# Optimization experiments

Hardware: AMD Instinct MI355X
Metric: run time of the kernel (lower is better)

## Reference

```python
import jax, jax.numpy as jnp
import numpy as np
import math

B, T, C = 4, 2048, 1024
H = 128            # num_heads
D = C // H         # head_dim = 8 (n_wires of the quantum device)


def setup_inputs() -> dict:
    key = jax.random.key(0)
    k1, k2, k3 = jax.random.split(key, 3)
    x = jax.random.normal(k1, (B, T, C), dtype=jnp.float32)
    # trainable RX angles: head_dim gates, each a scalar angle (tq.RX has_params=True)
    theta = jax.random.normal(k2, (D,), dtype=jnp.float32)
    # nn.Linear(C, C, bias=False) weight, torch layout [out, in]
    w_proj = jax.random.normal(k3, (C, C), dtype=jnp.float32) / math.sqrt(C)
    return {"x": x, "theta": theta, "w_proj": w_proj}


def _quantum_measure(xh, theta):
    # Circuit per head/token: start |0..0>, apply RX(x_j) on wire j (encoder
    # resets the state each call), then each of the D trainable RX(theta_g)
    # gates is broadcast over all wires. RX angles on one wire compose
    # additively, and <Z> after RX(phi)|0> == cos(phi).
    return jnp.cos(xh + jnp.sum(theta))  # [B, T, H, D]


def reference(x, theta, w_proj):
    xh = x.reshape(B, T, H, D)
    q = _quantum_measure(xh, theta)  # q == k == v (shared encoder + shared gates)
    # torch.matmul on [B,T,H,D]: batch dims (B,T) -> head-vs-head scores [B,T,H,H]
    scores = jnp.einsum('bthd,btgd->bthg', q, q) / math.sqrt(D)
    attn = jax.nn.softmax(scores, axis=-1)  # dropout: identity in eval
    out = jnp.einsum('bthg,btgd->bthd', attn, q).reshape(B, T, C)
    return out @ w_proj.T
```

## Files before the change

### kernel.cpp

```cpp
#include <hip/hip_runtime.h>
#include <hip/hip_bf16.h>
#include <stdint.h>

#define NB 4
#define NT 2048
#define NC 1024
#define NH 128
#define ND 8
#define NTOK (NB*NT)
#define GK 1024
#define GN 1024

typedef __attribute__((ext_vector_type(4))) float f32x4;
typedef __attribute__((ext_vector_type(8))) short bf16x8;
typedef __attribute__((ext_vector_type(8))) _Float16 f16x8;
typedef __attribute__((ext_vector_type(2))) _Float16 f16x2;
typedef __attribute__((ext_vector_type(4))) unsigned int u32x4;
typedef __attribute__((ext_vector_type(2))) unsigned int u32x2;
typedef unsigned int uint32;

#define GAMMA  0.71419167f
#define C1INV  1.4001844f

#define GLOAD_LDS16(g, l) \
  __builtin_amdgcn_global_load_lds((const __attribute__((address_space(1))) void*)(g), \
                                   (__attribute__((address_space(3))) void*)(l), 16, 0, 0)

__device__ __forceinline__ unsigned short f2bf(float f) {
  __bf16 b = (__bf16)f;
  return __builtin_bit_cast(unsigned short, b);
}
__device__ __forceinline__ f16x2 cvtpk_f16(float a, float b) {
  return __builtin_bit_cast(f16x2, __builtin_amdgcn_cvt_pkrtz(a, b));
}

__device__ __forceinline__ uint32 exp2pk(float a, float b) {
  f16x2 s = cvtpk_f16(a, b);
  const f16x2 MAGIC = {(_Float16)1536.0f, (_Float16)1536.0f};
  f16x2 t = s + MAGIC;
  f16x2 f = s - (t - MAGIC);
  const _Float16 k3 = (_Float16)(0.0555041f / 256.0f);
  const _Float16 k2 = (_Float16)(0.2402265f / 256.0f);
  const _Float16 k1 = (_Float16)(0.6931472f / 256.0f);
  const _Float16 k0 = (_Float16)(1.0f / 256.0f);
  const f16x2 P3 = {k3, k3}, P2 = {k2, k2}, P1 = {k1, k1}, P0 = {k0, k0};
  f16x2 p = P2 + f * P3;
  p = P1 + f * p;
  p = P0 + f * p;
  uint32 tb = __builtin_bit_cast(uint32, t);
  uint32 inj = ((((tb << 10) & 0xFC00FC00u) + 0x20002000u) & 0xFC00FC00u);
  return __builtin_bit_cast(uint32, p) + inj;
}

__global__ __launch_bounds__(256) void wconv_kernel(const float4* __restrict__ w,
                                                    ushort4* __restrict__ wb) {
  int i = blockIdx.x * 256 + threadIdx.x;
  float4 v = w[i];
  ushort4 o;
  o.x = f2bf(v.x); o.y = f2bf(v.y); o.z = f2bf(v.z); o.w = f2bf(v.w);
  wb[i] = o;
}

#define QTS 136

__global__ __launch_bounds__(256) void attn_kernel(const float* __restrict__ x,
                                                   const float* __restrict__ theta,
                                                   unsigned short* __restrict__ aout) {
  __shared__ __align__(16) unsigned short QT[4][8 * QTS];

  const int tid = (int)threadIdx.x;
  const int wid = tid >> 6;
  const int tok = blockIdx.x * 4 + wid;
  const int l = tid & 63;
  const int c = l & 15;
  const int t = l >> 4;

  float S = 0.f;
#pragma unroll
  for (int j = 0; j < ND; ++j) S += theta[j];

  u32x4 qf[8];
  unsigned short* qt = &QT[wid][0];
#pragma unroll
  for (int a = 0; a < 8; ++a) {
    float2 xv = *(const float2*)(x + (size_t)tok * NC + (16 * a + c) * ND + 2 * t);
    float q0 = GAMMA * __cosf(xv.x + S);
    float q1 = GAMMA * __cosf(xv.y + S);
    uint32 pk = __builtin_bit_cast(uint32, cvtpk_f16(q0, q1));
    qt[(2 * t) * QTS + 16 * a + c] = (unsigned short)(pk & 0xFFFFu);
    qt[(2 * t + 1) * QTS + 16 * a + c] = (unsigned short)(pk >> 16);
    qf[a].x = pk;
    qf[a].y = 0u; qf[a].z = 0u; qf[a].w = 0u;
  }

  u32x4 bff[4];
  {
    const int cm = (c < 8) ? c : 7;
    const bool isq = (c < 8);
    const uint32 onepair = 0x3C003C00u;
#pragma unroll
    for (int j = 0; j < 4; ++j) {
      u32x2 v0 = *(const u32x2*)&qt[cm * QTS + 32 * j + 4 * t];
      u32x2 v1 = *(const u32x2*)&qt[cm * QTS + 32 * j + 16 + 4 * t];
      bff[j].x = isq ? v0.x : onepair;
      bff[j].y = isq ? v0.y : onepair;
      bff[j].z = isq ? v1.x : onepair;
      bff[j].w = isq ? v1.y : onepair;
    }
  }

  const f32x4 z4 = {0.f, 0.f, 0.f, 0.f};
  unsigned short* orow = aout + (size_t)tok * NC;

#pragma unroll
  for (int b = 0; b < 8; ++b) {
    f32x4 o = z4;
#pragma unroll
    for (int j = 0; j < 4; ++j) {
      f32x4 sv0 = __builtin_amdgcn_mfma_f32_16x16x32_f16(
          __builtin_bit_cast(f16x8, qf[2 * j]), __builtin_bit_cast(f16x8, qf[b]),
          z4, 0, 0, 0);
      f32x4 sv1 = __builtin_amdgcn_mfma_f32_16x16x32_f16(
          __builtin_bit_cast(f16x8, qf[2 * j + 1]), __builtin_bit_cast(f16x8, qf[b]),
          z4, 0, 0, 0);
      u32x4 af;
      af.x = exp2pk(sv0[0], sv0[1]);
      af.y = exp2pk(sv0[2], sv0[3]);
      af.z = exp2pk(sv1[0], sv1[1]);
      af.w = exp2pk(sv1[2], sv1[3]);
      o = __builtin_amdgcn_mfma_f32_16x16x32_f16(
          __builtin_bit_cast(f16x8, af), __builtin_bit_cast(f16x8, bff[j]),
          o, 0, 0, 0);
    }
#pragma unroll
    for (int r = 0; r < 4; ++r) {
      float rs = __shfl_xor(o[r], 8, 64);
      float outv = o[r] * __builtin_amdgcn_rcpf(rs) * C1INV;
      if (c < 8)
        orow[(16 * b + 4 * t + r) * ND + c] = f2bf(outv);
    }
  }
}

#define BM 128
#define BN 128
#define BK 64

__global__ __launch_bounds__(512, 4) void gemm_kernel(const unsigned short* __restrict__ A,
                                                      const unsigned short* __restrict__ Bt,
                                                      float* __restrict__ C) {
  __shared__ __align__(16) unsigned short As[2][BM * BK];
  __shared__ __align__(16) unsigned short Bs[2][BN * BK];

  const int bm = blockIdx.x;
  const int bn = blockIdx.y;
  const int tid = (int)threadIdx.x;
  const int l = tid & 63;
  const int w = tid >> 6;
  const int wm = w >> 2;
  const int wn = w & 3;

  f32x4 acc[4][2] = {};

  const int srow = l >> 3;
  const int schk = (l & 7) ^ srow;
  const unsigned short* gA0 = A + (size_t)(bm * BM + 16 * w + srow) * GK + schk * 8;
  const unsigned short* gA1 = gA0 + 8 * GK;
  const unsigned short* gB0 = Bt + (size_t)(bn * BN + 16 * w + srow) * GK + schk * 8;
  const unsigned short* gB1 = gB0 + 8 * GK;

  const int fr = l & 15;
  const int kcb = l >> 4;
  const int fx = l & 7;

#define STAGE(nb)                                          \
  {                                                        \
    unsigned short* la = &As[nb][(16 * w) * BK];           \
    unsigned short* lb = &Bs[nb][(16 * w) * BK];           \
    GLOAD_LDS16(gA0, la);                                  \
    GLOAD_LDS16(gA1, la + 8 * BK);                         \
    GLOAD_LDS16(gB0, lb);                                  \
    GLOAD_LDS16(gB1, lb + 8 * BK);                         \
    gA0 += BK; gA1 += BK; gB0 += BK; gB1 += BK;            \
  }

  auto compute = [&](const unsigned short* as, const unsigned short* bs) {
#pragma unroll
    for (int s = 0; s < 2; ++s) {
      const int slot = ((4 * s + kcb) ^ fx) * 8;
      bf16x8 af[4], bfr[2];
#pragma unroll
      for (int i = 0; i < 4; ++i)
        af[i] = *reinterpret_cast<const bf16x8*>(&as[(64 * wm + 16 * i + fr) * BK + slot]);
#pragma unroll
      for (int j = 0; j < 2; ++j)
        bfr[j] = *reinterpret_cast<const bf16x8*>(&bs[(32 * wn + 16 * j + fr) * BK + slot]);
#pragma unroll
      for (int i = 0; i < 4; ++i)
#pragma unroll
        for (int j = 0; j < 2; ++j)
          acc[i][j] = __builtin_amdgcn_mfma_f32_16x16x32_bf16(af[i], bfr[j], acc[i][j], 0, 0, 0);
    }
  };

  STAGE(0);

  int buf = 0;
#pragma unroll 1
  for (int t = 0; t < 15; ++t) {
    STAGE(buf ^ 1);
    asm volatile("s_waitcnt vmcnt(4)" ::: "memory");
    __builtin_amdgcn_s_barrier();
    asm volatile("" ::: "memory");
    compute(&As[buf][0], &Bs[buf][0]);
    asm volatile("" ::: "memory");
    __builtin_amdgcn_s_barrier();
    asm volatile("" ::: "memory");
    buf ^= 1;
  }
  asm volatile("s_waitcnt vmcnt(0)" ::: "memory");
  __builtin_amdgcn_s_barrier();
  asm volatile("" ::: "memory");
  compute(&As[1][0], &Bs[1][0]);

  float* Cb = C + (size_t)(bm * BM + 64 * wm) * GN + bn * BN + 32 * wn;
  const int cr = (l >> 4) * 4;
  const int cc = l & 15;
#pragma unroll
  for (int i = 0; i < 4; ++i)
#pragma unroll
    for (int j = 0; j < 2; ++j)
#pragma unroll
      for (int r = 0; r < 4; ++r)
        Cb[(size_t)(16 * i + cr + r) * GN + 16 * j + cc] = acc[i][j][r];
#undef STAGE
}

extern "C" void kernel_launch(void* const* d_in, const int* in_sizes, int n_in,
                              void* d_out, int out_size, void* d_ws, size_t ws_size,
                              hipStream_t stream) {
  (void)in_sizes; (void)n_in; (void)out_size; (void)ws_size;
  const float* x = (const float*)d_in[0];
  const float* theta = (const float*)d_in[1];
  const float* wproj = (const float*)d_in[2];
  float* y = (float*)d_out;

  unsigned short* attn_out = (unsigned short*)d_ws;
  unsigned short* wb = (unsigned short*)((char*)d_ws + (size_t)NTOK * NC * 2);

  wconv_kernel<<<(NC * NC / 4) / 256, 256, 0, stream>>>((const float4*)wproj,
                                                        (ushort4*)wb);
  attn_kernel<<<NTOK / 4, 256, 0, stream>>>(x, theta, attn_out);
  dim3 grid(NTOK / BM, GN / BN);
  gemm_kernel<<<grid, 512, 0, stream>>>(attn_out, wb, y);
}
```

Baseline: 68.76 us.

## Process two tokens per wave in attention kernel with hoisted x loads

Each wave of the attention kernel now handles two tokens, 4096 apart, and issues the global x loads for both before any compute. This raises memory-level parallelism and halves the grid. The score MFMAs are grouped ahead of the exp2 polynomial and the output MFMAs so more independent work is in flight. A min-blocks launch bound of 3 is added. The cost is higher register pressure from holding both tokens' inputs, and the per-wave LDS scratch is reused across the two tokens.

```diff
diff --git a/kernel.cpp b/kernel.cpp
--- a/kernel.cpp
+++ b/kernel.cpp
@@ -63,29 +63,15 @@
 
 #define QTS 136
 
-__global__ __launch_bounds__(256) void attn_kernel(const float* __restrict__ x,
-                                                   const float* __restrict__ theta,
-                                                   unsigned short* __restrict__ aout) {
-  __shared__ __align__(16) unsigned short QT[4][8 * QTS];
-
-  const int tid = (int)threadIdx.x;
-  const int wid = tid >> 6;
-  const int tok = blockIdx.x * 4 + wid;
-  const int l = tid & 63;
-  const int c = l & 15;
-  const int t = l >> 4;
-
-  float S = 0.f;
-#pragma unroll
-  for (int j = 0; j < ND; ++j) S += theta[j];
-
+__device__ __forceinline__ void process_token(const float2* __restrict__ xv,
+                                              float S, unsigned short* qt,
+                                              unsigned short* __restrict__ orow,
+                                              int c, int t) {
   u32x4 qf[8];
-  unsigned short* qt = &QT[wid][0];
 #pragma unroll
   for (int a = 0; a < 8; ++a) {
-    float2 xv = *(const float2*)(x + (size_t)tok * NC + (16 * a + c) * ND + 2 * t);
-    float q0 = GAMMA * __cosf(xv.x + S);
-    float q1 = GAMMA * __cosf(xv.y + S);
+    float q0 = GAMMA * __cosf(xv[a].x + S);
+    float q1 = GAMMA * __cosf(xv[a].y + S);
     uint32 pk = __builtin_bit_cast(uint32, cvtpk_f16(q0, q1));
     qt[(2 * t) * QTS + 16 * a + c] = (unsigned short)(pk & 0xFFFFu);
     qt[(2 * t + 1) * QTS + 16 * a + c] = (unsigned short)(pk >> 16);
@@ -110,28 +96,33 @@
   }
 
   const f32x4 z4 = {0.f, 0.f, 0.f, 0.f};
-  unsigned short* orow = aout + (size_t)tok * NC;
 
 #pragma unroll
   for (int b = 0; b < 8; ++b) {
-    f32x4 o = z4;
+    f32x4 sv[8];
 #pragma unroll
     for (int j = 0; j < 4; ++j) {
-      f32x4 sv0 = __builtin_amdgcn_mfma_f32_16x16x32_f16(
+      sv[2 * j] = __builtin_amdgcn_mfma_f32_16x16x32_f16(
           __builtin_bit_cast(f16x8, qf[2 * j]), __builtin_bit_cast(f16x8, qf[b]),
           z4, 0, 0, 0);
-      f32x4 sv1 = __builtin_amdgcn_mfma_f32_16x16x32_f16(
+      sv[2 * j + 1] = __builtin_amdgcn_mfma_f32_16x16x32_f16(
           __builtin_bit_cast(f16x8, qf[2 * j + 1]), __builtin_bit_cast(f16x8, qf[b]),
           z4, 0, 0, 0);
-      u32x4 af;
-      af.x = exp2pk(sv0[0], sv0[1]);
-      af.y = exp2pk(sv0[2], sv0[3]);
-      af.z = exp2pk(sv1[0], sv1[1]);
-      af.w = exp2pk(sv1[2], sv1[3]);
+    }
+    u32x4 af[4];
+#pragma unroll
+    for (int j = 0; j < 4; ++j) {
+      af[j].x = exp2pk(sv[2 * j][0], sv[2 * j][1]);
+      af[j].y = exp2pk(sv[2 * j][2], sv[2 * j][3]);
+      af[j].z = exp2pk(sv[2 * j + 1][0], sv[2 * j + 1][1]);
+      af[j].w = exp2pk(sv[2 * j + 1][2], sv[2 * j + 1][3]);
+    }
+    f32x4 o = z4;
+#pragma unroll
+    for (int j = 0; j < 4; ++j)
       o = __builtin_amdgcn_mfma_f32_16x16x32_f16(
-          __builtin_bit_cast(f16x8, af), __builtin_bit_cast(f16x8, bff[j]),
+          __builtin_bit_cast(f16x8, af[j]), __builtin_bit_cast(f16x8, bff[j]),
           o, 0, 0, 0);
-    }
 #pragma unroll
     for (int r = 0; r < 4; ++r) {
       float rs = __shfl_xor(o[r], 8, 64);
@@ -140,6 +131,36 @@
         orow[(16 * b + 4 * t + r) * ND + c] = f2bf(outv);
     }
   }
+}
+
+__global__ __launch_bounds__(256, 3) void attn_kernel(const float* __restrict__ x,
+                                                      const float* __restrict__ theta,
+                                                      unsigned short* __restrict__ aout) {
+  __shared__ __align__(16) unsigned short QT[4][8 * QTS];
+
+  const int tid = (int)threadIdx.x;
+  const int wid = tid >> 6;
+  const int tok0 = blockIdx.x * 4 + wid;
+  const int tok1 = tok0 + 4096;
+  const int l = tid & 63;
+  const int c = l & 15;
+  const int t = l >> 4;
+
+  float S = 0.f;
+#pragma unroll
+  for (int j = 0; j < ND; ++j) S += theta[j];
+
+  float2 xv0[8], xv1[8];
+#pragma unroll
+  for (int a = 0; a < 8; ++a)
+    xv0[a] = *(const float2*)(x + (size_t)tok0 * NC + (16 * a + c) * ND + 2 * t);
+#pragma unroll
+  for (int a = 0; a < 8; ++a)
+    xv1[a] = *(const float2*)(x + (size_t)tok1 * NC + (16 * a + c) * ND + 2 * t);
+
+  unsigned short* qt = &QT[wid][0];
+  process_token(xv0, S, qt, aout + (size_t)tok0 * NC, c, t);
+  process_token(xv1, S, qt, aout + (size_t)tok1 * NC, c, t);
 }
 
 #define BM 128
@@ -195,6 +216,7 @@
 #pragma unroll
       for (int j = 0; j < 2; ++j)
         bfr[j] = *reinterpret_cast<const bf16x8*>(&bs[(32 * wn + 16 * j + fr) * BK + slot]);
+
 #pragma unroll
       for (int i = 0; i < 4; ++i)
 #pragma unroll
@@ -250,7 +272,7 @@
 
   wconv_kernel<<<(NC * NC / 4) / 256, 256, 0, stream>>>((const float4*)wproj,
                                                         (ushort4*)wb);
-  attn_kernel<<<NTOK / 4, 256, 0, stream>>>(x, theta, attn_out);
+  attn_kernel<<<NTOK / 8, 256, 0, stream>>>(x, theta, attn_out);
   dim3 grid(NTOK / BM, GN / BN);
   gemm_kernel<<<grid, 512, 0, stream>>>(attn_out, wb, y);
 }
```

New measurement: 66.95 us. 1.03x faster.
